# Kernel tuning notes

Measured on AMD Instinct MI355X. Metric: run time of the kernel, lower is better.

## Reference

```python
import jax, jax.numpy as jnp
import numpy as np

B, N, V, H, Z = 2048, 32, 10, 256, 64


def setup_inputs() -> dict:
    key = jax.random.key(0)
    ks = jax.random.split(key, 14)
    # strictly upper-triangular random DAG adjacency (topological order = vertex index)
    p = jax.random.uniform(ks[0], (B, N, N))
    tri = jnp.triu(jnp.ones((N, N), jnp.float32), k=1)
    adj = (p < 0.12).astype(jnp.float32) * tri
    node_types = jax.random.randint(ks[1], (B, N), 0, V).astype(jnp.int32)
    s = 0.05
    return dict(
        adj=adj,
        node_types=node_types,
        w_ih=jax.random.normal(ks[2], (V, 3 * H), jnp.float32) * s,
        w_hh=jax.random.normal(ks[3], (H, 3 * H), jnp.float32) * s,
        b_ih=jax.random.normal(ks[4], (3 * H,), jnp.float32) * s,
        b_hh=jax.random.normal(ks[5], (3 * H,), jnp.float32) * s,
        w_gate=jax.random.normal(ks[6], (H, H), jnp.float32) * s,
        b_gate=jax.random.normal(ks[7], (H,), jnp.float32) * s,
        w_map=jax.random.normal(ks[8], (H, H), jnp.float32) * s,
        w_mu=jax.random.normal(ks[9], (H, Z), jnp.float32) * s,
        b_mu=jax.random.normal(ks[10], (Z,), jnp.float32) * s,
        w_std=jax.random.normal(ks[11], (H, Z), jnp.float32) * s,
        b_std=jax.random.normal(ks[12], (Z,), jnp.float32) * s,
    )


def _gru_cell(x, h, w_ih, w_hh, b_ih, b_hh):
    # torch GRUCell math; weights stored [in, 3H]
    gi = x @ w_ih + b_ih  # [B, 3H]
    gh = h @ w_hh + b_hh
    i_r, i_z, i_n = jnp.split(gi, 3, axis=-1)
    h_r, h_z, h_n = jnp.split(gh, 3, axis=-1)
    r = jax.nn.sigmoid(i_r + h_r)
    z = jax.nn.sigmoid(i_z + h_z)
    n = jnp.tanh(i_n + r * h_n)
    return (1.0 - z) * n + z * h


def reference(adj, node_types, w_ih, w_hh, b_ih, b_hh, w_gate, b_gate, w_map,
              w_mu, b_mu, w_std, b_std):
    x_all = jax.nn.one_hot(node_types, V, dtype=adj.dtype)  # [B, N, V]
    hidden0 = jnp.zeros((B, N, H), adj.dtype)
    adj_cols = jnp.transpose(adj, (2, 0, 1))  # [N, B, N]; col v = predecessor mask of v
    x_seq = jnp.transpose(x_all, (1, 0, 2))   # [N, B, V]

    def step(hidden, inps):
        col, x, v = inps
        # gate(h_pred) * map(h_pred), summed over predecessors. map has no bias,
        # so non-predecessor (zero-masked) rows contribute exactly zero, matching
        # the padded-gather formulation in the original code.
        gm = jax.nn.sigmoid(hidden @ w_gate + b_gate) * (hidden @ w_map)  # [B, N, H]
        agg = jnp.einsum('bn,bnh->bh', col, gm)  # [B, H]; zero for v=0 (no preds)
        h_new = _gru_cell(x, agg, w_ih, w_hh, b_ih, b_hh)  # [B, H]
        hidden = jax.lax.dynamic_update_slice(hidden, h_new[:, None, :], (0, v, 0))
        return hidden, None

    hidden, _ = jax.lax.scan(step, hidden0, (adj_cols, x_seq, jnp.arange(N)))
    hg = hidden[:, -1, :]  # graph state = last vertex hidden
    mu = hg @ w_mu + b_mu
    sigma = hg @ w_std + b_std
    return (mu, sigma)
```

## Files before the change

kernel.cpp:

```cpp
#include <hip/hip_runtime.h>


#define BB 2048
#define NN 32
#define VV 10
#define HH 256
#define ZZ 64
#define BT 8
#define KC 8
#define NT1 48
#define NT2 32
#define WHH_ELEMS (NT1 * KC * 64 * 8)
#define WGM_ELEMS (NT2 * KC * 64 * 8)

typedef __attribute__((ext_vector_type(8))) short frag8;
typedef __attribute__((ext_vector_type(4))) float facc4;
typedef __attribute__((ext_vector_type(4))) unsigned short us4;

__device__ __forceinline__ float bf2f(unsigned short u) {
    unsigned int x = ((unsigned int)u) << 16;
    return __builtin_bit_cast(float, x);
}
__device__ __forceinline__ unsigned short f2bf(float f) {
    unsigned int x = __builtin_bit_cast(unsigned int, f);
    x += 0x7FFFu + ((x >> 16) & 1u);
    return (unsigned short)(x >> 16);
}
__device__ __forceinline__ float sigm(float x) { return 1.0f / (1.0f + __expf(-x)); }
__device__ __forceinline__ float ldv(const float* p, size_t i) { return p[i]; }
__device__ __forceinline__ float ldv(const unsigned short* p, size_t i) { return bf2f(p[i]); }
__device__ __forceinline__ void stv(float* p, size_t i, float v) { p[i] = v; }
__device__ __forceinline__ void stv(unsigned short* p, size_t i, float v) { p[i] = f2bf(v); }

__global__ void detect_dtype(const unsigned short* __restrict__ w, int* flag) {
    __shared__ int zc, bc;
    if (threadIdx.x == 0) { zc = 0; bc = 0; }
    __syncthreads();
    int z = 0, b = 0;
    for (int i = threadIdx.x; i < 2048; i += 256) {
        unsigned short lo = w[2 * i];
        if (lo == 0) z++;
        unsigned e = (lo >> 7) & 0xFFu;
        if (e >= 0x86u) b++;
    }
    atomicAdd(&zc, z); atomicAdd(&bc, b);
    __syncthreads();
    if (threadIdx.x == 0) *flag = (bc > 0 || zc > 512) ? 1 : 0;
}

template <typename T>
__global__ void repack_weights(const T* __restrict__ w_hh,
                               const T* __restrict__ w_gate,
                               const T* __restrict__ w_map,
                               const T* __restrict__ w_ih,
                               const T* __restrict__ b_ih,
                               unsigned short* __restrict__ whh_p,
                               unsigned short* __restrict__ wgm_p,
                               float* __restrict__ wihG,
                               const int* __restrict__ flag, int want) {
    if (*flag != want) return;
    int t = blockIdx.x * blockDim.x + threadIdx.x;
    int lane = t & 63;
    int frag = t >> 6;
    int kbase = (lane >> 4) * 8;
    if (frag < NT1 * KC) {
        int jt = frag / KC, kc = frag % KC;
        int col = jt * 16 + (lane & 15);
        unsigned short* dst = whh_p + ((size_t)frag * 64 + lane) * 8;
        #pragma unroll
        for (int j = 0; j < 8; ++j)
            dst[j] = f2bf(ldv(w_hh, (size_t)(kc * 32 + kbase + j) * 768 + col));
    } else if (frag < (NT1 + NT2) * KC) {
        int f2 = frag - NT1 * KC;
        int jt = f2 / KC, kc = f2 % KC;
        int col = jt * 16 + (lane & 15);
        unsigned short* dst = wgm_p + ((size_t)f2 * 64 + lane) * 8;
        #pragma unroll
        for (int j = 0; j < 8; ++j) {
            int k = kc * 32 + kbase + j;
            dst[j] = f2bf((col < HH) ? ldv(w_gate, (size_t)k * HH + col)
                                     : ldv(w_map, (size_t)k * HH + (col - HH)));
        }
    } else {
        int idx = t - (NT1 + NT2) * KC * 64;
        if (idx < VV * 768) {
            int c = idx % 768;
            wihG[idx] = ldv(w_ih, (size_t)idx) + ldv(b_ih, (size_t)c);
        }
    }
}

template <typename T>
__global__ __launch_bounds__(1024, 4) void vae_main(
    const T* __restrict__ adj,
    const int* __restrict__ ntypes,
    const T* __restrict__ b_hh,
    const T* __restrict__ b_gate,
    const T* __restrict__ w_mu,
    const T* __restrict__ b_mu,
    const T* __restrict__ w_std,
    const T* __restrict__ b_std,
    const unsigned short* __restrict__ whh_p,
    const unsigned short* __restrict__ wgm_p,
    const float* __restrict__ wihG,
    T* __restrict__ out,
    const int* __restrict__ flag, int want)
{
    if (*flag != want) return;

    __shared__ __align__(16) unsigned short gmAll[BT][NN][HH];
    __shared__ __align__(16) unsigned short aggbf[16][264];
    __shared__ __align__(16) unsigned short hnew[16][264];
    __shared__ unsigned int  amask[BT][NN];
    __shared__ int           ntva[BT][NN];
    __shared__ __align__(16) float bhhL[768];
    __shared__ float bgL[HH];

    float* const aggA = (float*)&aggbf[8][0];
    float* const aggB = (float*)&hnew[8][0];

    const int tid  = threadIdx.x;
    const int lane = tid & 63;
    const int w    = tid >> 6;
    const int b0   = blockIdx.x * BT;

    const frag8* whh8 = (const frag8*)whh_p;
    const frag8* wgm8 = (const frag8*)wgm_p;

    if (tid < 256) {
        int bi = tid >> 5, vv = tid & 31;
        unsigned m = 0;
        for (int n = 0; n < NN; ++n)
            if (ldv(adj, ((size_t)(b0 + bi) * NN + n) * NN + vv) != 0.0f) m |= (1u << n);
        amask[bi][vv] = m;
    } else if (tid < 512) {
        int idx = tid - 256;
        int bi = idx >> 5, vv = idx & 31;
        ntva[bi][vv] = ntypes[(b0 + bi) * NN + vv];
    }
    for (int i = tid; i < 768; i += 1024) bhhL[i] = ldv(b_hh, i);
    if (tid < HH) bgL[tid] = ldv(b_gate, tid);

    frag8 wG[KC], wM[KC];
    {
        const frag8* pG = wgm8 + (size_t)w * (KC * 64) + lane;
        const frag8* pM = wgm8 + (size_t)(w + 16) * (KC * 64) + lane;
        #pragma unroll
        for (int kc = 0; kc < KC; ++kc) { wG[kc] = pG[kc * 64]; wM[kc] = pM[kc * 64]; }
    }
    __syncthreads();

    for (int v = 0; v < NN; ++v) {
        if (w < BT) {
            const int bi = w;
            const int h4 = lane * 4;
            unsigned m = amask[bi][v];
            float a0 = 0.f, a1 = 0.f, a2 = 0.f, a3 = 0.f;
            const unsigned short* rb = &gmAll[bi][0][0] + h4;
            while (m) {
                const int n0 = __builtin_ctz(m); m &= m - 1;
                const us4 g0 = *(const us4*)(rb + n0 * HH);
                if (m) {
                    const int n1 = __builtin_ctz(m); m &= m - 1;
                    const us4 g1 = *(const us4*)(rb + n1 * HH);
                    a0 += bf2f(g0.x) + bf2f(g1.x);
                    a1 += bf2f(g0.y) + bf2f(g1.y);
                    a2 += bf2f(g0.z) + bf2f(g1.z);
                    a3 += bf2f(g0.w) + bf2f(g1.w);
                } else {
                    a0 += bf2f(g0.x); a1 += bf2f(g0.y);
                    a2 += bf2f(g0.z); a3 += bf2f(g0.w);
                }
            }
            float* ap = (bi < 4) ? (aggA + bi * 256) : (aggB + (bi - 4) * 256);
            *(float4*)(ap + h4) = make_float4(a0, a1, a2, a3);
            ushort4 ab; ab.x = f2bf(a0); ab.y = f2bf(a1); ab.z = f2bf(a2); ab.w = f2bf(a3);
            *(ushort4*)&aggbf[bi][h4] = ab;
        }
        __syncthreads();

        {
            const int t = w;
            const int col = t * 16 + (lane & 15);
            const int q = lane >> 4;
            float xr[4], xz[4], xn[4];
            if (q < 2) {
                #pragma unroll
                for (int i = 0; i < 4; ++i) {
                    const float* wr = wihG + (size_t)ntva[4 * q + i][v] * 768 + col;
                    xr[i] = wr[0]; xz[i] = wr[256]; xn[i] = wr[512];
                }
            }
            frag8 afrag[KC];
            #pragma unroll
            for (int kc = 0; kc < KC; ++kc)
                afrag[kc] = *(const frag8*)&aggbf[lane & 15][kc * 32 + (lane >> 4) * 8];

            facc4 aR = {0.f, 0.f, 0.f, 0.f};
            facc4 aZ = {0.f, 0.f, 0.f, 0.f};
            facc4 aN = {0.f, 0.f, 0.f, 0.f};
            const frag8* pR = whh8 + (size_t)(t     ) * (KC * 64) + lane;
            const frag8* pZ = whh8 + (size_t)(t + 16) * (KC * 64) + lane;
            const frag8* pN = whh8 + (size_t)(t + 32) * (KC * 64) + lane;
            #pragma unroll
            for (int kc = 0; kc < KC; ++kc) {
                aR = __builtin_amdgcn_mfma_f32_16x16x32_bf16(afrag[kc], pR[kc * 64], aR, 0, 0, 0);
                aZ = __builtin_amdgcn_mfma_f32_16x16x32_bf16(afrag[kc], pZ[kc * 64], aZ, 0, 0, 0);
                aN = __builtin_amdgcn_mfma_f32_16x16x32_bf16(afrag[kc], pN[kc * 64], aN, 0, 0, 0);
            }
            if (q < 2) {
                const float bhr = bhhL[col], bhz = bhhL[col + 256], bhn = bhhL[col + 512];
                const float* ap = (q == 0) ? aggA : aggB;
                #pragma unroll
                for (int i = 0; i < 4; ++i) {
                    const float r = sigm(xr[i] + aR[i] + bhr);
                    const float z = sigm(xz[i] + aZ[i] + bhz);
                    const float n = tanhf(xn[i] + r * (aN[i] + bhn));
                    hnew[4 * q + i][col] = f2bf((1.f - z) * n + z * ap[i * 256 + col]);
                }
            }
        }
        __syncthreads();

        {
            frag8 hfrag[KC];
            #pragma unroll
            for (int kc = 0; kc < KC; ++kc)
                hfrag[kc] = *(const frag8*)&hnew[lane & 15][kc * 32 + (lane >> 4) * 8];

            facc4 aG = {0.f, 0.f, 0.f, 0.f};
            facc4 aM = {0.f, 0.f, 0.f, 0.f};
            #pragma unroll
            for (int kc = 0; kc < KC; ++kc) {
                aG = __builtin_amdgcn_mfma_f32_16x16x32_bf16(hfrag[kc], wG[kc], aG, 0, 0, 0);
                aM = __builtin_amdgcn_mfma_f32_16x16x32_bf16(hfrag[kc], wM[kc], aM, 0, 0, 0);
            }
            const int col = w * 16 + (lane & 15);
            const int q = lane >> 4;
            if (q < 2) {
                const float bg = bgL[col];
                #pragma unroll
                for (int i = 0; i < 4; ++i)
                    gmAll[4 * q + i][v][col] = f2bf(sigm(aG[i] + bg) * aM[i]);
            }
        }
        __syncthreads();
    }

    {
        const int bi = w >> 1, half = w & 1, z = lane;
        float am = 0.f, as = 0.f;
        const int h0 = half * 128;
        #pragma unroll 4
        for (int h = h0; h < h0 + 128; ++h) {
            const float hv = bf2f(hnew[bi][h]);
            am += hv * ldv(w_mu, (size_t)h * ZZ + z);
            as += hv * ldv(w_std, (size_t)h * ZZ + z);
        }
        float* sc = (bi < 4) ? (aggA + bi * 256) : (aggB + (bi - 4) * 256);
        sc[half * 64 + z]       = am;
        sc[128 + half * 64 + z] = as;
    }
    __syncthreads();
    if (w < BT) {
        const int bi = w, z = lane;
        const float* sc = (bi < 4) ? (aggA + bi * 256) : (aggB + (bi - 4) * 256);
        const float am = sc[z] + sc[64 + z] + ldv(b_mu, z);
        const float as = sc[128 + z] + sc[192 + z] + ldv(b_std, z);
        stv(out, (size_t)(b0 + bi) * ZZ + z, am);
        stv(out, (size_t)BB * ZZ + (size_t)(b0 + bi) * ZZ + z, as);
    }
}

extern "C" void kernel_launch(void* const* d_in, const int* in_sizes, int n_in,
                              void* d_out, int out_size, void* d_ws, size_t ws_size,
                              hipStream_t stream)
{
    unsigned short* whh_p = (unsigned short*)d_ws;
    unsigned short* wgm_p = whh_p + WHH_ELEMS;
    float* wihG = (float*)(wgm_p + WGM_ELEMS);

    size_t flag_off = (ws_size >= 8) ? ((ws_size - 4) & ~(size_t)3) : 0;
    int* flag = (int*)((char*)d_ws + flag_off);

    detect_dtype<<<dim3(1), 256, 0, stream>>>((const unsigned short*)d_in[2], flag);

    repack_weights<float><<<dim3(190), 256, 0, stream>>>(
        (const float*)d_in[3], (const float*)d_in[6], (const float*)d_in[8],
        (const float*)d_in[2], (const float*)d_in[4],
        whh_p, wgm_p, wihG, flag, 1);
    repack_weights<unsigned short><<<dim3(190), 256, 0, stream>>>(
        (const unsigned short*)d_in[3], (const unsigned short*)d_in[6],
        (const unsigned short*)d_in[8], (const unsigned short*)d_in[2],
        (const unsigned short*)d_in[4],
        whh_p, wgm_p, wihG, flag, 0);

    vae_main<float><<<dim3(BB / BT), 1024, 0, stream>>>(
        (const float*)d_in[0], (const int*)d_in[1],
        (const float*)d_in[5], (const float*)d_in[7],
        (const float*)d_in[9], (const float*)d_in[10],
        (const float*)d_in[11], (const float*)d_in[12],
        whh_p, wgm_p, wihG, (float*)d_out, flag, 1);
    vae_main<unsigned short><<<dim3(BB / BT), 1024, 0, stream>>>(
        (const unsigned short*)d_in[0], (const int*)d_in[1],
        (const unsigned short*)d_in[5], (const unsigned short*)d_in[7],
        (const unsigned short*)d_in[9], (const unsigned short*)d_in[10],
        (const unsigned short*)d_in[11], (const unsigned short*)d_in[12],
        whh_p, wgm_p, wihG, (unsigned short*)d_out, flag, 0);
}
```

Before: 541.9 us.

## Spill gated-message history to global scratch and double batch tile per block

Moves the per-vertex gate*map message history from a large LDS array into per-block global scratch slabs, keeping only the latest row in LDS and writing it out with nontemporal stores one step later. This frees LDS so each block can handle 16 graphs with 512 threads, doubling the MFMA work per wave and removing the idle half-waves in the old GRU epilogue. In exchange, predecessor gathers now read from global memory (L2/HBM latency on the serial critical path). Launches may be split into chunks when the workspace is too small for all slabs.

```diff
diff --git a/kernel.cpp b/kernel.cpp
--- a/kernel.cpp
+++ b/kernel.cpp
@@ -6,12 +6,16 @@
 #define VV 10
 #define HH 256
 #define ZZ 64
-#define BT 8
+#define BT 16
 #define KC 8
 #define NT1 48
 #define NT2 32
 #define WHH_ELEMS (NT1 * KC * 64 * 8)
 #define WGM_ELEMS (NT2 * KC * 64 * 8)
+#define WIH_BYTES (VV * 768 * 4)
+#define GM_BYTE_OFF ((WHH_ELEMS + WGM_ELEMS) * 2 + WIH_BYTES)
+#define SLAB_ELEMS (BT * NN * HH)
+#define SLAB_BYTES (SLAB_ELEMS * 2)
 
 typedef __attribute__((ext_vector_type(8))) short frag8;
 typedef __attribute__((ext_vector_type(4))) float facc4;
@@ -31,6 +35,12 @@
 __device__ __forceinline__ float ldv(const unsigned short* p, size_t i) { return bf2f(p[i]); }
 __device__ __forceinline__ void stv(float* p, size_t i, float v) { p[i] = v; }
 __device__ __forceinline__ void stv(unsigned short* p, size_t i, float v) { p[i] = f2bf(v); }
+__device__ __forceinline__ us4 ntld4(const unsigned short* p) {
+    return __builtin_nontemporal_load((const us4*)p);
+}
+__device__ __forceinline__ void ntst4(unsigned short* p, us4 v) {
+    __builtin_nontemporal_store(v, (us4*)p);
+}
 
 __global__ void detect_dtype(const unsigned short* __restrict__ w, int* flag) {
     __shared__ int zc, bc;
@@ -91,7 +101,7 @@
 }
 
 template <typename T>
-__global__ __launch_bounds__(1024, 4) void vae_main(
+__global__ __launch_bounds__(512, 2) void vae_main(
     const T* __restrict__ adj,
     const int* __restrict__ ntypes,
     const T* __restrict__ b_hh,
@@ -103,12 +113,15 @@
     const unsigned short* __restrict__ whh_p,
     const unsigned short* __restrict__ wgm_p,
     const float* __restrict__ wihG,
+    unsigned short* __restrict__ gm_base,
     T* __restrict__ out,
+    int b_start,
     const int* __restrict__ flag, int want)
 {
     if (*flag != want) return;
 
-    __shared__ __align__(16) unsigned short gmAll[BT][NN][HH];
+    __shared__ __align__(16) unsigned short gmrow[BT][HH];
+    __shared__ __align__(16) float agg[BT][HH];
     __shared__ __align__(16) unsigned short aggbf[16][264];
     __shared__ __align__(16) unsigned short hnew[16][264];
     __shared__ unsigned int  amask[BT][NN];
@@ -116,109 +129,115 @@
     __shared__ __align__(16) float bhhL[768];
     __shared__ float bgL[HH];
 
-    float* const aggA = (float*)&aggbf[8][0];
-    float* const aggB = (float*)&hnew[8][0];
-
     const int tid  = threadIdx.x;
     const int lane = tid & 63;
     const int w    = tid >> 6;
-    const int b0   = blockIdx.x * BT;
+    const int b0   = b_start + blockIdx.x * BT;
+
+    unsigned short* gms = gm_base + (size_t)blockIdx.x * SLAB_ELEMS;
 
     const frag8* whh8 = (const frag8*)whh_p;
     const frag8* wgm8 = (const frag8*)wgm_p;
 
-    if (tid < 256) {
+    {
         int bi = tid >> 5, vv = tid & 31;
         unsigned m = 0;
         for (int n = 0; n < NN; ++n)
             if (ldv(adj, ((size_t)(b0 + bi) * NN + n) * NN + vv) != 0.0f) m |= (1u << n);
         amask[bi][vv] = m;
-    } else if (tid < 512) {
-        int idx = tid - 256;
-        int bi = idx >> 5, vv = idx & 31;
         ntva[bi][vv] = ntypes[(b0 + bi) * NN + vv];
     }
-    for (int i = tid; i < 768; i += 1024) bhhL[i] = ldv(b_hh, i);
+    for (int i = tid; i < 768; i += 512) bhhL[i] = ldv(b_hh, i);
     if (tid < HH) bgL[tid] = ldv(b_gate, tid);
 
-    frag8 wG[KC], wM[KC];
+    frag8 wG0[KC], wG1[KC], wM0[KC], wM1[KC];
     {
-        const frag8* pG = wgm8 + (size_t)w * (KC * 64) + lane;
-        const frag8* pM = wgm8 + (size_t)(w + 16) * (KC * 64) + lane;
+        const frag8* p0 = wgm8 + (size_t)(w     ) * (KC * 64) + lane;
+        const frag8* p1 = wgm8 + (size_t)(w +  8) * (KC * 64) + lane;
+        const frag8* p2 = wgm8 + (size_t)(w + 16) * (KC * 64) + lane;
+        const frag8* p3 = wgm8 + (size_t)(w + 24) * (KC * 64) + lane;
         #pragma unroll
-        for (int kc = 0; kc < KC; ++kc) { wG[kc] = pG[kc * 64]; wM[kc] = pM[kc * 64]; }
+        for (int kc = 0; kc < KC; ++kc) {
+            wG0[kc] = p0[kc * 64]; wG1[kc] = p1[kc * 64];
+            wM0[kc] = p2[kc * 64]; wM1[kc] = p3[kc * 64];
+        }
     }
     __syncthreads();
 
     for (int v = 0; v < NN; ++v) {
-        if (w < BT) {
-            const int bi = w;
+        {
             const int h4 = lane * 4;
-            unsigned m = amask[bi][v];
-            float a0 = 0.f, a1 = 0.f, a2 = 0.f, a3 = 0.f;
-            const unsigned short* rb = &gmAll[bi][0][0] + h4;
-            while (m) {
-                const int n0 = __builtin_ctz(m); m &= m - 1;
-                const us4 g0 = *(const us4*)(rb + n0 * HH);
-                if (m) {
-                    const int n1 = __builtin_ctz(m); m &= m - 1;
-                    const us4 g1 = *(const us4*)(rb + n1 * HH);
-                    a0 += bf2f(g0.x) + bf2f(g1.x);
-                    a1 += bf2f(g0.y) + bf2f(g1.y);
-                    a2 += bf2f(g0.z) + bf2f(g1.z);
-                    a3 += bf2f(g0.w) + bf2f(g1.w);
-                } else {
-                    a0 += bf2f(g0.x); a1 += bf2f(g0.y);
-                    a2 += bf2f(g0.z); a3 += bf2f(g0.w);
+            #pragma unroll
+            for (int s = 0; s < 2; ++s) {
+                const int bi = 2 * w + s;
+                unsigned m0 = amask[bi][v];
+                unsigned m  = (v > 0) ? (m0 & ~(1u << (v - 1))) : m0;
+                float a0 = 0.f, a1 = 0.f, a2 = 0.f, a3 = 0.f;
+                const unsigned short* rb = gms + (size_t)bi * NN * HH + h4;
+                while (m) {
+                    const int n0 = __builtin_ctz(m); m &= m - 1;
+                    const us4 g0 = ntld4(rb + (size_t)n0 * HH);
+                    if (m) {
+                        const int n1 = __builtin_ctz(m); m &= m - 1;
+                        const us4 g1 = ntld4(rb + (size_t)n1 * HH);
+                        a0 += bf2f(g0.x) + bf2f(g1.x);
+                        a1 += bf2f(g0.y) + bf2f(g1.y);
+                        a2 += bf2f(g0.z) + bf2f(g1.z);
+                        a3 += bf2f(g0.w) + bf2f(g1.w);
+                    } else {
+                        a0 += bf2f(g0.x); a1 += bf2f(g0.y);
+                        a2 += bf2f(g0.z); a3 += bf2f(g0.w);
+                    }
+                }
+                if (v > 0) {
+                    const us4 gr = *(const us4*)&gmrow[bi][h4];
+                    if ((m0 >> (v - 1)) & 1u) {
+                        a0 += bf2f(gr.x); a1 += bf2f(gr.y);
+                        a2 += bf2f(gr.z); a3 += bf2f(gr.w);
+                    }
+                    ntst4(gms + ((size_t)bi * NN + (v - 1)) * HH + h4, gr);
+                }
+                *(float4*)&agg[bi][h4] = make_float4(a0, a1, a2, a3);
+                ushort4 ab; ab.x = f2bf(a0); ab.y = f2bf(a1); ab.z = f2bf(a2); ab.w = f2bf(a3);
+                *(ushort4*)&aggbf[bi][h4] = ab;
+            }
+        }
+        __syncthreads();
+
+        {
+            frag8 afrag[KC];
+            #pragma unroll
+            for (int kc = 0; kc < KC; ++kc)
+                afrag[kc] = *(const frag8*)&aggbf[lane & 15][kc * 32 + (lane >> 4) * 8];
+
+            #pragma unroll
+            for (int s = 0; s < 2; ++s) {
+                const int t = w + 8 * s;
+                facc4 aR = {0.f, 0.f, 0.f, 0.f};
+                facc4 aZ = {0.f, 0.f, 0.f, 0.f};
+                facc4 aN = {0.f, 0.f, 0.f, 0.f};
+                const frag8* pR = whh8 + (size_t)(t     ) * (KC * 64) + lane;
+                const frag8* pZ = whh8 + (size_t)(t + 16) * (KC * 64) + lane;
+                const frag8* pN = whh8 + (size_t)(t + 32) * (KC * 64) + lane;
+                #pragma unroll
+                for (int kc = 0; kc < KC; ++kc) {
+                    aR = __builtin_amdgcn_mfma_f32_16x16x32_bf16(afrag[kc], pR[kc * 64], aR, 0, 0, 0);
+                    aZ = __builtin_amdgcn_mfma_f32_16x16x32_bf16(afrag[kc], pZ[kc * 64], aZ, 0, 0, 0);
+                    aN = __builtin_amdgcn_mfma_f32_16x16x32_bf16(afrag[kc], pN[kc * 64], aN, 0, 0, 0);
+                }
+                const int col = t * 16 + (lane & 15);
+                const int q = lane >> 4;
+                const float bhr = bhhL[col], bhz = bhhL[col + 256], bhn = bhhL[col + 512];
+                #pragma unroll
+                for (int i = 0; i < 4; ++i) {
+                    const int bi = 4 * q + i;
+                    const float* wr = wihG + (size_t)ntva[bi][v] * 768 + col;
+                    const float r = sigm(wr[0]   + aR[i] + bhr);
+                    const float z = sigm(wr[256] + aZ[i] + bhz);
+                    const float n = tanhf(wr[512] + r * (aN[i] + bhn));
+                    hnew[bi][col] = f2bf((1.f - z) * n + z * agg[bi][col]);
                 }
             }
-            float* ap = (bi < 4) ? (aggA + bi * 256) : (aggB + (bi - 4) * 256);
-            *(float4*)(ap + h4) = make_float4(a0, a1, a2, a3);
-            ushort4 ab; ab.x = f2bf(a0); ab.y = f2bf(a1); ab.z = f2bf(a2); ab.w = f2bf(a3);
-            *(ushort4*)&aggbf[bi][h4] = ab;
-        }
-        __syncthreads();
-
-        {
-            const int t = w;
-            const int col = t * 16 + (lane & 15);
-            const int q = lane >> 4;
-            float xr[4], xz[4], xn[4];
-            if (q < 2) {
-                #pragma unroll
-                for (int i = 0; i < 4; ++i) {
-                    const float* wr = wihG + (size_t)ntva[4 * q + i][v] * 768 + col;
-                    xr[i] = wr[0]; xz[i] = wr[256]; xn[i] = wr[512];
-                }
-            }
-            frag8 afrag[KC];
-            #pragma unroll
-            for (int kc = 0; kc < KC; ++kc)
-                afrag[kc] = *(const frag8*)&aggbf[lane & 15][kc * 32 + (lane >> 4) * 8];
-
-            facc4 aR = {0.f, 0.f, 0.f, 0.f};
-            facc4 aZ = {0.f, 0.f, 0.f, 0.f};
-            facc4 aN = {0.f, 0.f, 0.f, 0.f};
-            const frag8* pR = whh8 + (size_t)(t     ) * (KC * 64) + lane;
-            const frag8* pZ = whh8 + (size_t)(t + 16) * (KC * 64) + lane;
-            const frag8* pN = whh8 + (size_t)(t + 32) * (KC * 64) + lane;
-            #pragma unroll
-            for (int kc = 0; kc < KC; ++kc) {
-                aR = __builtin_amdgcn_mfma_f32_16x16x32_bf16(afrag[kc], pR[kc * 64], aR, 0, 0, 0);
-                aZ = __builtin_amdgcn_mfma_f32_16x16x32_bf16(afrag[kc], pZ[kc * 64], aZ, 0, 0, 0);
-                aN = __builtin_amdgcn_mfma_f32_16x16x32_bf16(afrag[kc], pN[kc * 64], aN, 0, 0, 0);
-            }
-            if (q < 2) {
-                const float bhr = bhhL[col], bhz = bhhL[col + 256], bhn = bhhL[col + 512];
-                const float* ap = (q == 0) ? aggA : aggB;
-                #pragma unroll
-                for (int i = 0; i < 4; ++i) {
-                    const float r = sigm(xr[i] + aR[i] + bhr);
-                    const float z = sigm(xz[i] + aZ[i] + bhz);
-                    const float n = tanhf(xn[i] + r * (aN[i] + bhn));
-                    hnew[4 * q + i][col] = f2bf((1.f - z) * n + z * ap[i * 256 + col]);
-                }
-            }
         }
         __syncthreads();
 
@@ -228,47 +247,42 @@
             for (int kc = 0; kc < KC; ++kc)
                 hfrag[kc] = *(const frag8*)&hnew[lane & 15][kc * 32 + (lane >> 4) * 8];
 
-            facc4 aG = {0.f, 0.f, 0.f, 0.f};
-            facc4 aM = {0.f, 0.f, 0.f, 0.f};
+            facc4 aG0 = {0.f, 0.f, 0.f, 0.f};
+            facc4 aG1 = {0.f, 0.f, 0.f, 0.f};
+            facc4 aM0 = {0.f, 0.f, 0.f, 0.f};
+            facc4 aM1 = {0.f, 0.f, 0.f, 0.f};
             #pragma unroll
             for (int kc = 0; kc < KC; ++kc) {
-                aG = __builtin_amdgcn_mfma_f32_16x16x32_bf16(hfrag[kc], wG[kc], aG, 0, 0, 0);
-                aM = __builtin_amdgcn_mfma_f32_16x16x32_bf16(hfrag[kc], wM[kc], aM, 0, 0, 0);
+                aG0 = __builtin_amdgcn_mfma_f32_16x16x32_bf16(hfrag[kc], wG0[kc], aG0, 0, 0, 0);
+                aG1 = __builtin_amdgcn_mfma_f32_16x16x32_bf16(hfrag[kc], wG1[kc], aG1, 0, 0, 0);
+                aM0 = __builtin_amdgcn_mfma_f32_16x16x32_bf16(hfrag[kc], wM0[kc], aM0, 0, 0, 0);
+                aM1 = __builtin_amdgcn_mfma_f32_16x16x32_bf16(hfrag[kc], wM1[kc], aM1, 0, 0, 0);
             }
-            const int col = w * 16 + (lane & 15);
             const int q = lane >> 4;
-            if (q < 2) {
-                const float bg = bgL[col];
-                #pragma unroll
-                for (int i = 0; i < 4; ++i)
-                    gmAll[4 * q + i][v][col] = f2bf(sigm(aG[i] + bg) * aM[i]);
+            const int c0 = w * 16 + (lane & 15);
+            const int c1 = (w + 8) * 16 + (lane & 15);
+            const float bg0 = bgL[c0], bg1 = bgL[c1];
+            #pragma unroll
+            for (int i = 0; i < 4; ++i) {
+                gmrow[4 * q + i][c0] = f2bf(sigm(aG0[i] + bg0) * aM0[i]);
+                gmrow[4 * q + i][c1] = f2bf(sigm(aG1[i] + bg1) * aM1[i]);
             }
         }
         __syncthreads();
     }
 
-    {
-        const int bi = w >> 1, half = w & 1, z = lane;
+    #pragma unroll
+    for (int s = 0; s < 2; ++s) {
+        const int bi = 2 * w + s, z = lane;
         float am = 0.f, as = 0.f;
-        const int h0 = half * 128;
         #pragma unroll 4
-        for (int h = h0; h < h0 + 128; ++h) {
+        for (int h = 0; h < HH; ++h) {
             const float hv = bf2f(hnew[bi][h]);
             am += hv * ldv(w_mu, (size_t)h * ZZ + z);
             as += hv * ldv(w_std, (size_t)h * ZZ + z);
         }
-        float* sc = (bi < 4) ? (aggA + bi * 256) : (aggB + (bi - 4) * 256);
-        sc[half * 64 + z]       = am;
-        sc[128 + half * 64 + z] = as;
-    }
-    __syncthreads();
-    if (w < BT) {
-        const int bi = w, z = lane;
-        const float* sc = (bi < 4) ? (aggA + bi * 256) : (aggB + (bi - 4) * 256);
-        const float am = sc[z] + sc[64 + z] + ldv(b_mu, z);
-        const float as = sc[128 + z] + sc[192 + z] + ldv(b_std, z);
-        stv(out, (size_t)(b0 + bi) * ZZ + z, am);
-        stv(out, (size_t)BB * ZZ + (size_t)(b0 + bi) * ZZ + z, as);
+        stv(out, (size_t)(b0 + bi) * ZZ + z, am + ldv(b_mu, z));
+        stv(out, (size_t)BB * ZZ + (size_t)(b0 + bi) * ZZ + z, as + ldv(b_std, z));
     }
 }
 
@@ -279,9 +293,15 @@
     unsigned short* whh_p = (unsigned short*)d_ws;
     unsigned short* wgm_p = whh_p + WHH_ELEMS;
     float* wihG = (float*)(wgm_p + WGM_ELEMS);
+    unsigned short* gm_base = (unsigned short*)((char*)d_ws + GM_BYTE_OFF);
 
     size_t flag_off = (ws_size >= 8) ? ((ws_size - 4) & ~(size_t)3) : 0;
     int* flag = (int*)((char*)d_ws + flag_off);
+
+    long long avail = (long long)flag_off - (long long)GM_BYTE_OFF;
+    int cb = (int)(avail / SLAB_BYTES);
+    if (cb < 1) cb = 1;
+    if (cb > BB / BT) cb = BB / BT;
 
     detect_dtype<<<dim3(1), 256, 0, stream>>>((const unsigned short*)d_in[2], flag);
 
@@ -295,16 +315,20 @@
         (const unsigned short*)d_in[4],
         whh_p, wgm_p, wihG, flag, 0);
 
-    vae_main<float><<<dim3(BB / BT), 1024, 0, stream>>>(
-        (const float*)d_in[0], (const int*)d_in[1],
-        (const float*)d_in[5], (const float*)d_in[7],
-        (const float*)d_in[9], (const float*)d_in[10],
-        (const float*)d_in[11], (const float*)d_in[12],
-        whh_p, wgm_p, wihG, (float*)d_out, flag, 1);
-    vae_main<unsigned short><<<dim3(BB / BT), 1024, 0, stream>>>(
-        (const unsigned short*)d_in[0], (const int*)d_in[1],
-        (const unsigned short*)d_in[5], (const unsigned short*)d_in[7],
-        (const unsigned short*)d_in[9], (const unsigned short*)d_in[10],
-        (const unsigned short*)d_in[11], (const unsigned short*)d_in[12],
-        whh_p, wgm_p, wihG, (unsigned short*)d_out, flag, 0);
-}
+    const int nblk = BB / BT;
+    for (int blk0 = 0; blk0 < nblk; blk0 += cb) {
+        int g = nblk - blk0; if (g > cb) g = cb;
+        vae_main<float><<<dim3(g), 512, 0, stream>>>(
+            (const float*)d_in[0], (const int*)d_in[1],
+            (const float*)d_in[5], (const float*)d_in[7],
+            (const float*)d_in[9], (const float*)d_in[10],
+            (const float*)d_in[11], (const float*)d_in[12],
+            whh_p, wgm_p, wihG, gm_base, (float*)d_out, blk0 * BT, flag, 1);
+        vae_main<unsigned short><<<dim3(g), 512, 0, stream>>>(
+            (const unsigned short*)d_in[0], (const int*)d_in[1],
+            (const unsigned short*)d_in[5], (const unsigned short*)d_in[7],
+            (const unsigned short*)d_in[9], (const unsigned short*)d_in[10],
+            (const unsigned short*)d_in[11], (const unsigned short*)d_in[12],
+            whh_p, wgm_p, wihG, gm_base, (unsigned short*)d_out, blk0 * BT, flag, 0);
+    }
+}
```

After: 729.2 us. 34.5% more time.
